# Kernel tuning notes

Measured on AMD Instinct MI355X. Metric: run time of the kernel, lower is better.

The kernel has to match this reference:

```python
import jax, jax.numpy as jnp
import numpy as np

B, N, K, C, C_OUT = 8, 4096, 16, 192, 192
BN_EPS = 1e-5


def setup_inputs() -> dict:
    key = jax.random.key(0)
    k1, k2, k3, k4 = jax.random.split(key, 4)
    x = jax.random.normal(k1, (B, N, C), dtype=jnp.float32)
    edge_index = jax.random.randint(k2, (B, N, K), 0, N)
    # Linear(2C -> C_out): store weight as [2C, C_out] (transposed torch layout)
    lim = 1.0 / np.sqrt(2 * C)
    W = jax.random.uniform(k3, (2 * C, C_OUT), minval=-lim, maxval=lim, dtype=jnp.float32)
    b = jax.random.uniform(k4, (C_OUT,), minval=-lim, maxval=lim, dtype=jnp.float32)
    gamma = jnp.ones((C_OUT,), dtype=jnp.float32)
    beta = jnp.zeros((C_OUT,), dtype=jnp.float32)
    return {"x": x, "W": W, "b": b, "gamma": gamma, "beta": beta, "edge_index": edge_index}


def reference(x, W, b, gamma, beta, edge_index):
    Bb, Nn, Cc = x.shape
    # gather neighbor features: neighbors[b,n,k,:] = x[b, edge_index[b,n,k], :]
    batch_idx = jnp.arange(Bb)[:, None, None]          # [B,1,1]
    neighbors = x[batch_idx, edge_index]               # [B,N,K,C]
    # max-relative aggregation: max_k (x_j - x_i)
    agg = jnp.max(neighbors - x[:, :, None, :], axis=2)  # [B,N,C]
    h = jnp.concatenate([x, agg], axis=-1).reshape(Bb * Nn, 2 * Cc)
    # Linear
    y = h @ W + b                                      # [B*N, C_out]
    # BatchNorm1d (training-mode forward: batch stats, biased variance)
    mean = jnp.mean(y, axis=0)
    var = jnp.var(y, axis=0)
    y = (y - mean) * jax.lax.rsqrt(var + BN_EPS) * gamma + beta
    # exact (erf) GELU, torch default
    y = jax.nn.gelu(y, approximate=False)
    return y.reshape(Bb, Nn, -1)
```

## Files before the change

### kernel.cpp

```cpp
#include <hip/hip_runtime.h>
#include <math.h>

#define BDIM 8
#define NDIM 4096
#define KNBR 16
#define CDIM 192
#define COUT 192
#define TWO_C 384
#define ROWS (BDIM * NDIM)
#define BN_EPS 1e-5f

#define BM 64
#define HS 392
#define KSTEPS 12
#define NTILES 12

typedef __attribute__((ext_vector_type(8))) short short8;
typedef __attribute__((ext_vector_type(4))) float f32x4;

__device__ __forceinline__ float bf2f(unsigned short u) {
    unsigned int x = ((unsigned int)u) << 16;
    return __builtin_bit_cast(float, x);
}
__device__ __forceinline__ unsigned short f2bf(float f) {
    unsigned int u = __builtin_bit_cast(unsigned int, f);
    u += 0x7FFFu + ((u >> 16) & 1u);
    return (unsigned short)(u >> 16);
}
__device__ __forceinline__ float gelu_exact(float v) {
    return 0.5f * v * (1.0f + erff(v * 0.70710678118654752440f));
}

#define CVT_BLK0 37
__global__ __launch_bounds__(256)
void prep(const float* __restrict__ x, const float* __restrict__ W,
          unsigned short* __restrict__ xb, unsigned short* __restrict__ Wtp,
          float* __restrict__ stats) {
    const int bid = blockIdx.x;
    const int t   = threadIdx.x;
    if (bid < 36) {
        const int tid = bid * 256 + t;
        const int ks = tid / (NTILES * 64);
        const int r  = tid % (NTILES * 64);
        const int nt = r / 64;
        const int l  = r % 64;
        const int k0 = ks * 32 + ((l >> 4) << 3);
        const int c  = nt * 16 + (l & 15);
        short8 o;
#pragma unroll
        for (int j = 0; j < 8; ++j)
            o[j] = (short)f2bf(W[(size_t)(k0 + j) * COUT + c]);
        *(short8*)(Wtp + (size_t)tid * 8) = o;
        return;
    }
    if (bid == 36) {
        for (int s = t; s < 2 * COUT; s += 256) stats[s] = 0.0f;
        return;
    }
    const int i = (bid - CVT_BLK0) * 256 + t;
    const float4* p = (const float4*)(x + (size_t)i * 8);
    const float4 a = p[0], b = p[1];
    short8 o;
    o[0] = (short)f2bf(a.x); o[1] = (short)f2bf(a.y);
    o[2] = (short)f2bf(a.z); o[3] = (short)f2bf(a.w);
    o[4] = (short)f2bf(b.x); o[5] = (short)f2bf(b.y);
    o[6] = (short)f2bf(b.z); o[7] = (short)f2bf(b.w);
    *(short8*)(xb + (size_t)i * 8) = o;
}

__global__ __launch_bounds__(512)
void mrconv_mfma(const unsigned short* __restrict__ xb,
                 const unsigned short* __restrict__ Wtp,
                 const int*   __restrict__ edge,
                 unsigned short* __restrict__ y,
                 float* __restrict__ stats)
{
    __shared__ unsigned short h[BM * HS];
    __shared__ int eidx[BM * KNBR];

    const int t     = threadIdx.x;
    const int bid   = blockIdx.x;
    const int batch = bid & 7;
    const int tile  = bid >> 3;
    const int row0  = tile * BM;

    const unsigned short* xbb = xb + (size_t)batch * NDIM * CDIM;
    const int* eb = edge + ((size_t)batch * NDIM + row0) * KNBR;

    for (int i = t; i < BM * KNBR; i += 512) eidx[i] = eb[i];
    __syncthreads();

    for (int it = 0; it < 3; ++it) {
        const int idx = it * 512 + t;
        const int cc  = idx % 24;
        const int ln  = idx / 24;
        const short8 xi8 = *(const short8*)(xbb + (size_t)(row0 + ln) * CDIM + cc * 8);
        float mx[8];
#pragma unroll
        for (int q = 0; q < 8; ++q) mx[q] = -INFINITY;
#pragma unroll
        for (int k = 0; k < KNBR; ++k) {
            const int j = eidx[ln * KNBR + k];
            const short8 xj8 = *(const short8*)(xbb + (size_t)j * CDIM + cc * 8);
#pragma unroll
            for (int q = 0; q < 8; ++q)
                mx[q] = fmaxf(mx[q], bf2f((unsigned short)xj8[q]));
        }
        short8 a8;
#pragma unroll
        for (int q = 0; q < 8; ++q)
            a8[q] = (short)f2bf(mx[q] - bf2f((unsigned short)xi8[q]));
        *(short8*)&h[ln * HS + cc * 8]        = xi8;
        *(short8*)&h[ln * HS + CDIM + cc * 8] = a8;
    }
    __syncthreads();

    const int wv   = t >> 6;
    const int lane = t & 63;
    const int wr   = wv >> 2;
    const int wc   = wv & 3;
    const int lrow = lane & 15;
    const int lk   = (lane >> 4) << 3;

    f32x4 acc[2][3];
#pragma unroll
    for (int mt = 0; mt < 2; ++mt)
#pragma unroll
        for (int nt = 0; nt < 3; ++nt)
            acc[mt][nt] = (f32x4){0.f, 0.f, 0.f, 0.f};

    for (int ks = 0; ks < KSTEPS; ++ks) {
        short8 bfr[3], afr[2];
#pragma unroll
        for (int nt = 0; nt < 3; ++nt) {
            const int ng = wc * 3 + nt;
            bfr[nt] = *(const short8*)(Wtp + (size_t)((ks * NTILES + ng) * 64 + lane) * 8);
        }
#pragma unroll
        for (int mt = 0; mt < 2; ++mt)
            afr[mt] = *(const short8*)&h[((wr * 2 + mt) * 16 + lrow) * HS + ks * 32 + lk];
#pragma unroll
        for (int mt = 0; mt < 2; ++mt)
#pragma unroll
            for (int nt = 0; nt < 3; ++nt)
                acc[mt][nt] = __builtin_amdgcn_mfma_f32_16x16x32_bf16(
                    afr[mt], bfr[nt], acc[mt][nt], 0, 0, 0);
    }

    const size_t growbase = (size_t)batch * NDIM + row0;
    const int rj = (lane >> 4) << 2;
#pragma unroll
    for (int mt = 0; mt < 2; ++mt) {
#pragma unroll
        for (int nt = 0; nt < 3; ++nt) {
            const int col = wc * 48 + nt * 16 + lrow;
#pragma unroll
            for (int j = 0; j < 4; ++j) {
                const size_t rr = growbase + (wr * 2 + mt) * 16 + rj + j;
                y[rr * COUT + col] = f2bf(acc[mt][nt][j]);
            }
        }
    }

    float psums[3], psqs[3];
#pragma unroll
    for (int nt = 0; nt < 3; ++nt) {
        float s = 0.f, q = 0.f;
#pragma unroll
        for (int mt = 0; mt < 2; ++mt)
#pragma unroll
            for (int j = 0; j < 4; ++j) {
                const float v = acc[mt][nt][j];
                s += v; q += v * v;
            }
        s += __shfl_xor(s, 16); s += __shfl_xor(s, 32);
        q += __shfl_xor(q, 16); q += __shfl_xor(q, 32);
        psums[nt] = s; psqs[nt] = q;
    }
    __syncthreads();
    float* psum = (float*)h;
    float* psq  = psum + 2 * COUT;
    if (lane < 16) {
#pragma unroll
        for (int nt = 0; nt < 3; ++nt) {
            const int col = wc * 48 + nt * 16 + lane;
            psum[wr * COUT + col] = psums[nt];
            psq [wr * COUT + col] = psqs[nt];
        }
    }
    __syncthreads();
    if (t < COUT) {
        atomicAdd(&stats[t],        psum[t] + psum[COUT + t]);
        atomicAdd(&stats[COUT + t], psq[t]  + psq[COUT + t]);
    }
}

__global__ __launch_bounds__(256)
void bn_gelu(const unsigned short* __restrict__ y,
             const float* __restrict__ stats,
             const float* __restrict__ gamma,
             const float* __restrict__ beta,
             float* __restrict__ out)
{
    __shared__ float sscale[COUT];
    __shared__ float sshift[COUT];
    const int t = threadIdx.x;
    if (t < COUT) {
        const float inv  = 1.0f / (float)ROWS;
        const float mean = stats[t] * inv;
        const float var  = stats[COUT + t] * inv - mean * mean;
        const float rstd = rsqrtf(var + BN_EPS);
        const float sc   = rstd * gamma[t];
        sscale[t] = sc;
        sshift[t] = beta[t] - mean * sc;
    }
    __syncthreads();

    const int i = blockIdx.x * 256 + t;
    short8 v = *(const short8*)(y + (size_t)i * 8);
    const int c0 = (i % 24) * 8;
    float4 o0, o1;
    o0.x = gelu_exact(fmaf(bf2f((unsigned short)v[0]), sscale[c0 + 0], sshift[c0 + 0]));
    o0.y = gelu_exact(fmaf(bf2f((unsigned short)v[1]), sscale[c0 + 1], sshift[c0 + 1]));
    o0.z = gelu_exact(fmaf(bf2f((unsigned short)v[2]), sscale[c0 + 2], sshift[c0 + 2]));
    o0.w = gelu_exact(fmaf(bf2f((unsigned short)v[3]), sscale[c0 + 3], sshift[c0 + 3]));
    o1.x = gelu_exact(fmaf(bf2f((unsigned short)v[4]), sscale[c0 + 4], sshift[c0 + 4]));
    o1.y = gelu_exact(fmaf(bf2f((unsigned short)v[5]), sscale[c0 + 5], sshift[c0 + 5]));
    o1.z = gelu_exact(fmaf(bf2f((unsigned short)v[6]), sscale[c0 + 6], sshift[c0 + 6]));
    o1.w = gelu_exact(fmaf(bf2f((unsigned short)v[7]), sscale[c0 + 7], sshift[c0 + 7]));
    float4* po = (float4*)(out + (size_t)i * 8);
    po[0] = o0;
    po[1] = o1;
}

extern "C" void kernel_launch(void* const* d_in, const int* in_sizes, int n_in,
                              void* d_out, int out_size, void* d_ws, size_t ws_size,
                              hipStream_t stream) {
    const float* x     = (const float*)d_in[0];
    const float* W     = (const float*)d_in[1];
    const float* gamma = (const float*)d_in[3];
    const float* beta  = (const float*)d_in[4];
    const int*   edge  = (const int*)d_in[5];
    float* out = (float*)d_out;

    unsigned short* Wtp  = (unsigned short*)d_ws;
    float* stats = (float*)(Wtp + (size_t)KSTEPS * NTILES * 64 * 8);
    unsigned short* y16  = (unsigned short*)(stats + 2 * COUT);
    unsigned short* xb16 = y16 + (size_t)ROWS * COUT;

    prep<<<dim3(CVT_BLK0 + ROWS * CDIM / 8 / 256), dim3(256), 0, stream>>>(x, W, xb16, Wtp, stats);
    mrconv_mfma<<<dim3(ROWS / BM), dim3(512), 0, stream>>>(xb16, Wtp, edge, y16, stats);
    bn_gelu<<<dim3(ROWS * COUT / 8 / 256), dim3(256), 0, stream>>>(y16, stats, gamma, beta, out);
}
```

Before: 50.56 us.

## Gather neighbors from LDS-resident channel chunks and stream GEMM operands directly

The neighbor max-aggregation moves into its own kernel. Each block loads one 8-channel slice of a whole batch of x into shared memory as bf16, so the 16 random neighbor reads hit LDS instead of global memory. The result is written in a channel-chunked layout that the GEMM kernel reads directly as MFMA A fragments, and the x half of the A operand is converted from fp32 on the fly instead of going through a separate bf16 copy. This drops the x-to-bf16 prep pass and the scattered global gathers, at the cost of re-reading edge indices per channel chunk and loading A fragments from global memory without LDS staging.

```diff
diff --git a/kernel.cpp b/kernel.cpp
--- a/kernel.cpp
+++ b/kernel.cpp
@@ -6,21 +6,18 @@
 #define KNBR 16
 #define CDIM 192
 #define COUT 192
-#define TWO_C 384
 #define ROWS (BDIM * NDIM)
 #define BN_EPS 1e-5f
-
-#define BM 64
-#define HS 392
 #define KSTEPS 12
 #define NTILES 12
+#define CH 24
 
 typedef __attribute__((ext_vector_type(8))) short short8;
 typedef __attribute__((ext_vector_type(4))) float f32x4;
 
 __device__ __forceinline__ float bf2f(unsigned short u) {
-    unsigned int x = ((unsigned int)u) << 16;
-    return __builtin_bit_cast(float, x);
+    unsigned int v = ((unsigned int)u) << 16;
+    return __builtin_bit_cast(float, v);
 }
 __device__ __forceinline__ unsigned short f2bf(float f) {
     unsigned int u = __builtin_bit_cast(unsigned int, f);
@@ -31,15 +28,23 @@
     return 0.5f * v * (1.0f + erff(v * 0.70710678118654752440f));
 }
 
-#define CVT_BLK0 37
-__global__ __launch_bounds__(256)
-void prep(const float* __restrict__ x, const float* __restrict__ W,
-          unsigned short* __restrict__ xb, unsigned short* __restrict__ Wtp,
-          float* __restrict__ stats) {
-    const int bid = blockIdx.x;
-    const int t   = threadIdx.x;
-    if (bid < 36) {
-        const int tid = bid * 256 + t;
+__global__ __launch_bounds__(512)
+void gather_agg(const float* __restrict__ x, const float* __restrict__ W,
+                const int* __restrict__ edge,
+                unsigned short* __restrict__ aggcm,
+                unsigned short* __restrict__ Wtp,
+                float* __restrict__ stats)
+{
+    __shared__ unsigned short xck[NDIM * 8];
+
+    const int t    = threadIdx.x;
+    const int bid  = blockIdx.x;
+    const int b    = bid & 7;
+    const int half = (bid >> 3) & 1;
+    const int cc   = bid >> 4;
+
+    if (bid < 18) {
+        const int tid = bid * 512 + t;
         const int ks = tid / (NTILES * 64);
         const int r  = tid % (NTILES * 64);
         const int nt = r / 64;
@@ -51,76 +56,74 @@
         for (int j = 0; j < 8; ++j)
             o[j] = (short)f2bf(W[(size_t)(k0 + j) * COUT + c]);
         *(short8*)(Wtp + (size_t)tid * 8) = o;
-        return;
-    }
-    if (bid == 36) {
-        for (int s = t; s < 2 * COUT; s += 256) stats[s] = 0.0f;
-        return;
-    }
-    const int i = (bid - CVT_BLK0) * 256 + t;
-    const float4* p = (const float4*)(x + (size_t)i * 8);
-    const float4 a = p[0], b = p[1];
-    short8 o;
-    o[0] = (short)f2bf(a.x); o[1] = (short)f2bf(a.y);
-    o[2] = (short)f2bf(a.z); o[3] = (short)f2bf(a.w);
-    o[4] = (short)f2bf(b.x); o[5] = (short)f2bf(b.y);
-    o[6] = (short)f2bf(b.z); o[7] = (short)f2bf(b.w);
-    *(short8*)(xb + (size_t)i * 8) = o;
+    }
+    if (bid == 18 && t < 2 * COUT) stats[t] = 0.0f;
+
+    const float* xb = x + (size_t)b * NDIM * CDIM + cc * 8;
+#pragma unroll
+    for (int s = 0; s < 8; ++s) {
+        const int n = s * 512 + t;
+        const float4* p = (const float4*)(xb + (size_t)n * CDIM);
+        const float4 a = p[0], c4 = p[1];
+        short8 o;
+        o[0] = (short)f2bf(a.x);  o[1] = (short)f2bf(a.y);
+        o[2] = (short)f2bf(a.z);  o[3] = (short)f2bf(a.w);
+        o[4] = (short)f2bf(c4.x); o[5] = (short)f2bf(c4.y);
+        o[6] = (short)f2bf(c4.z); o[7] = (short)f2bf(c4.w);
+        *(short8*)&xck[n * 8] = o;
+    }
+    __syncthreads();
+
+    const int n0 = half * 2048;
+#pragma unroll
+    for (int s = 0; s < 4; ++s) {
+        const int n = n0 + s * 512 + t;
+        const int4* ep = (const int4*)(edge + ((size_t)b * NDIM + n) * KNBR);
+        const int4 e0 = ep[0], e1 = ep[1], e2 = ep[2], e3 = ep[3];
+        const int js[16] = {e0.x, e0.y, e0.z, e0.w, e1.x, e1.y, e1.z, e1.w,
+                            e2.x, e2.y, e2.z, e2.w, e3.x, e3.y, e3.z, e3.w};
+        float mx[8];
+#pragma unroll
+        for (int q = 0; q < 8; ++q) mx[q] = -INFINITY;
+#pragma unroll
+        for (int k = 0; k < KNBR; ++k) {
+            const short8 v = *(const short8*)&xck[js[k] * 8];
+#pragma unroll
+            for (int q = 0; q < 8; ++q)
+                mx[q] = fmaxf(mx[q], bf2f((unsigned short)v[q]));
+        }
+        const short8 xi = *(const short8*)&xck[n * 8];
+        short8 a8;
+#pragma unroll
+        for (int q = 0; q < 8; ++q)
+            a8[q] = (short)f2bf(mx[q] - bf2f((unsigned short)xi[q]));
+        *(short8*)(aggcm + (((size_t)b * CH + cc) * NDIM + n) * 8) = a8;
+    }
 }
 
 __global__ __launch_bounds__(512)
-void mrconv_mfma(const unsigned short* __restrict__ xb,
-                 const unsigned short* __restrict__ Wtp,
-                 const int*   __restrict__ edge,
-                 unsigned short* __restrict__ y,
-                 float* __restrict__ stats)
+void gemm_stats(const float* __restrict__ x,
+                const unsigned short* __restrict__ aggcm,
+                const unsigned short* __restrict__ Wtp,
+                unsigned short* __restrict__ y,
+                float* __restrict__ stats)
 {
-    __shared__ unsigned short h[BM * HS];
-    __shared__ int eidx[BM * KNBR];
-
-    const int t     = threadIdx.x;
-    const int bid   = blockIdx.x;
-    const int batch = bid & 7;
-    const int tile  = bid >> 3;
-    const int row0  = tile * BM;
-
-    const unsigned short* xbb = xb + (size_t)batch * NDIM * CDIM;
-    const int* eb = edge + ((size_t)batch * NDIM + row0) * KNBR;
-
-    for (int i = t; i < BM * KNBR; i += 512) eidx[i] = eb[i];
-    __syncthreads();
-
-    for (int it = 0; it < 3; ++it) {
-        const int idx = it * 512 + t;
-        const int cc  = idx % 24;
-        const int ln  = idx / 24;
-        const short8 xi8 = *(const short8*)(xbb + (size_t)(row0 + ln) * CDIM + cc * 8);
-        float mx[8];
-#pragma unroll
-        for (int q = 0; q < 8; ++q) mx[q] = -INFINITY;
-#pragma unroll
-        for (int k = 0; k < KNBR; ++k) {
-            const int j = eidx[ln * KNBR + k];
-            const short8 xj8 = *(const short8*)(xbb + (size_t)j * CDIM + cc * 8);
-#pragma unroll
-            for (int q = 0; q < 8; ++q)
-                mx[q] = fmaxf(mx[q], bf2f((unsigned short)xj8[q]));
-        }
-        short8 a8;
-#pragma unroll
-        for (int q = 0; q < 8; ++q)
-            a8[q] = (short)f2bf(mx[q] - bf2f((unsigned short)xi8[q]));
-        *(short8*)&h[ln * HS + cc * 8]        = xi8;
-        *(short8*)&h[ln * HS + CDIM + cc * 8] = a8;
-    }
-    __syncthreads();
+    __shared__ float psum[2 * COUT];
+    __shared__ float psq[2 * COUT];
+
+    const int t    = threadIdx.x;
+    const int bid  = blockIdx.x;
+    const int b    = bid & 7;
+    const int tile = bid >> 3;
+    const int row0 = tile * 64;
 
     const int wv   = t >> 6;
     const int lane = t & 63;
     const int wr   = wv >> 2;
     const int wc   = wv & 3;
     const int lrow = lane & 15;
-    const int lk   = (lane >> 4) << 3;
+    const int lg   = lane >> 4;
+    const int lk   = lg << 3;
 
     f32x4 acc[2][3];
 #pragma unroll
@@ -132,13 +135,30 @@
     for (int ks = 0; ks < KSTEPS; ++ks) {
         short8 bfr[3], afr[2];
 #pragma unroll
-        for (int nt = 0; nt < 3; ++nt) {
-            const int ng = wc * 3 + nt;
-            bfr[nt] = *(const short8*)(Wtp + (size_t)((ks * NTILES + ng) * 64 + lane) * 8);
-        }
-#pragma unroll
-        for (int mt = 0; mt < 2; ++mt)
-            afr[mt] = *(const short8*)&h[((wr * 2 + mt) * 16 + lrow) * HS + ks * 32 + lk];
+        for (int nt = 0; nt < 3; ++nt)
+            bfr[nt] = *(const short8*)(Wtp + (size_t)((ks * NTILES + wc * 3 + nt) * 64 + lane) * 8);
+        if (ks < 6) {
+#pragma unroll
+            for (int mt = 0; mt < 2; ++mt) {
+                const int row = row0 + (wr * 2 + mt) * 16 + lrow;
+                const float* xr = x + ((size_t)b * NDIM + row) * CDIM + ks * 32 + lk;
+                const float4 a = ((const float4*)xr)[0];
+                const float4 c4 = ((const float4*)xr)[1];
+                short8 o;
+                o[0] = (short)f2bf(a.x);  o[1] = (short)f2bf(a.y);
+                o[2] = (short)f2bf(a.z);  o[3] = (short)f2bf(a.w);
+                o[4] = (short)f2bf(c4.x); o[5] = (short)f2bf(c4.y);
+                o[6] = (short)f2bf(c4.z); o[7] = (short)f2bf(c4.w);
+                afr[mt] = o;
+            }
+        } else {
+            const int cg = (ks - 6) * 4 + lg;
+#pragma unroll
+            for (int mt = 0; mt < 2; ++mt) {
+                const int row = row0 + (wr * 2 + mt) * 16 + lrow;
+                afr[mt] = *(const short8*)(aggcm + (((size_t)b * CH + cg) * NDIM + row) * 8);
+            }
+        }
 #pragma unroll
         for (int mt = 0; mt < 2; ++mt)
 #pragma unroll
@@ -147,8 +167,8 @@
                     afr[mt], bfr[nt], acc[mt][nt], 0, 0, 0);
     }
 
-    const size_t growbase = (size_t)batch * NDIM + row0;
-    const int rj = (lane >> 4) << 2;
+    const size_t growbase = (size_t)b * NDIM + row0;
+    const int rj = lg << 2;
 #pragma unroll
     for (int mt = 0; mt < 2; ++mt) {
 #pragma unroll
@@ -178,8 +198,6 @@
         psums[nt] = s; psqs[nt] = q;
     }
     __syncthreads();
-    float* psum = (float*)h;
-    float* psq  = psum + 2 * COUT;
     if (lane < 16) {
 #pragma unroll
         for (int nt = 0; nt < 3; ++nt) {
@@ -243,12 +261,12 @@
     const int*   edge  = (const int*)d_in[5];
     float* out = (float*)d_out;
 
-    unsigned short* Wtp  = (unsigned short*)d_ws;
+    unsigned short* Wtp   = (unsigned short*)d_ws;
     float* stats = (float*)(Wtp + (size_t)KSTEPS * NTILES * 64 * 8);
-    unsigned short* y16  = (unsigned short*)(stats + 2 * COUT);
-    unsigned short* xb16 = y16 + (size_t)ROWS * COUT;
-
-    prep<<<dim3(CVT_BLK0 + ROWS * CDIM / 8 / 256), dim3(256), 0, stream>>>(x, W, xb16, Wtp, stats);
-    mrconv_mfma<<<dim3(ROWS / BM), dim3(512), 0, stream>>>(xb16, Wtp, edge, y16, stats);
+    unsigned short* y16   = (unsigned short*)(stats + 2 * COUT);
+    unsigned short* aggcm = y16 + (size_t)ROWS * COUT;
+
+    gather_agg<<<dim3(384), dim3(512), 0, stream>>>(x, W, edge, aggcm, Wtp, stats);
+    gemm_stats<<<dim3(512), dim3(512), 0, stream>>>(x, aggcm, Wtp, y16, stats);
     bn_gelu<<<dim3(ROWS * COUT / 8 / 256), dim3(256), 0, stream>>>(y16, stats, gamma, beta, out);
 }
```

After: 67.45 us. 1.33x slower.
